# Performance work log

Measured on AMD Instinct MI355X. Metric: run time of the kernel, lower is better.

Reference implementation:

```python
import jax, jax.numpy as jnp
import numpy as np

NC = 6            # CPAB tessellation cells (tess_size=6, zero_boundary=True)
DIM = NC - 1      # theta dimension = 5
SIG_LEN = 2048
CHANNELS = 3
BATCH = 256
FC_IN = 64 * 168  # flattened net_part1 output for signal_len=2048
NUM_SCALING = 0   # N in transform_data_ss
EPS_BN = 1e-5


def _cpab_basis():
    """QR null-space basis of the CPAB continuity + zero-boundary constraints.
    Params ordered [a_1,b_1,...,a_NC,b_NC]; v(x)=a_c x + b_c on cell c."""
    nc = NC
    L = np.zeros((nc + 1, 2 * nc))
    for k in range(1, nc):  # continuity at internal knots x_k = k/nc
        xk = k / nc
        L[k - 1, 2 * (k - 1)] = xk
        L[k - 1, 2 * (k - 1) + 1] = 1.0
        L[k - 1, 2 * k] = -xk
        L[k - 1, 2 * k + 1] = -1.0
    L[nc - 1, 1] = 1.0        # v(0) = 0  -> b_1 = 0
    L[nc, 2 * (nc - 1)] = 1.0  # v(1) = 0 -> a_nc + b_nc = 0
    L[nc, 2 * nc - 1] = 1.0
    Q, _ = np.linalg.qr(L.T, mode='complete')
    return np.ascontiguousarray(Q[:, nc + 1:]).astype(np.float32)  # (12, 5)


def _conv1d(x, w, b):
    y = jax.lax.conv_general_dilated(x, w, (1,), 'VALID',
                                     dimension_numbers=('NCH', 'OIH', 'NCH'))
    return y + b[None, :, None]


def _maxpool1d(x, k, s):
    return jax.lax.reduce_window(x, -jnp.inf, jax.lax.max, (1, 1, k), (1, 1, s), 'VALID')


def _bn(x, g, b, m, v):  # eval-mode BatchNorm1d
    return (x - m[None, :, None]) * (g / jnp.sqrt(v + EPS_BN))[None, :, None] + b[None, :, None]


def _integrate(x, A):
    """Exact CPAB 1D flow integration over t=1 with cell-crossing handling.
    x: (B, n) points in [0,1]; A: (B, NC, 2) per-cell (a, b). Monotone
    trajectories cross at most NC-1 boundaries -> fixed NC+1 iterations."""
    a_all, b_all = A[:, :, 0], A[:, :, 1]
    t = jnp.ones_like(x)
    for _ in range(NC + 1):
        c = jnp.clip(jnp.floor(x * NC).astype(jnp.int32), 0, NC - 1)
        a = jnp.take_along_axis(a_all, c, axis=1)
        b = jnp.take_along_axis(b_all, c, axis=1)
        v = a * x + b
        xb = jnp.where(v >= 0, (c + 1).astype(x.dtype) / NC, c.astype(x.dtype) / NC)
        big_a = jnp.abs(a) > 1e-8
        a_s = jnp.where(big_a, a, 1.0)
        z = x + b / a_s        # shifted coord: x(t) = z*exp(a t) - b/a
        zb = xb + b / a_s
        ratio = zb / jnp.where(jnp.abs(z) > 1e-12, z, 1e-12)
        t_exp = jnp.log(jnp.maximum(ratio, 1e-12)) / a_s
        v_s = jnp.where(jnp.abs(v) > 1e-12, v, 1.0)
        t_lin = (xb - x) / v_s
        thit = jnp.where(big_a, t_exp, t_lin)
        valid = (jnp.abs(v) > 1e-12) & (thit > 0) & (jnp.where(big_a, ratio, 1.0) > 0)
        thit = jnp.where(valid, thit, jnp.inf)
        tau = jnp.minimum(t, thit)
        x_new = jnp.where(big_a, z * jnp.exp(a * tau) - (z - x), x + b * tau)
        hit = thit <= t
        nudge = jnp.where(v >= 0, 1e-6, -1e-6)  # push into next cell
        x = jnp.clip(jnp.where(hit, xb + nudge, x_new), 0.0, 1.0)
        t = jnp.maximum(t - tau, 0.0)
    return x


def _interp1d(data, pos):
    """data: (B, L, C); pos: (B, n) in [0,1] -> (B, n, C) linear interpolation."""
    Lw = data.shape[1]
    p = jnp.clip(pos, 0.0, 1.0) * (Lw - 1)
    x0 = jnp.clip(jnp.floor(p).astype(jnp.int32), 0, Lw - 2)
    w = (p - x0.astype(p.dtype))[:, :, None]
    d0 = jnp.take_along_axis(data, x0[:, :, None], axis=1)
    d1 = jnp.take_along_axis(data, (x0 + 1)[:, :, None], axis=1)
    return d0 * (1.0 - w) + d1 * w


def _transform_data_ss(data, theta, basis, outsize, N):
    """CPAB scaling-and-squaring warp of data (B, L, C) by theta (B, DIM)."""
    Bsz = theta.shape[0]
    A = (theta @ basis.T).reshape(Bsz, NC, 2) / (2.0 ** N)
    grid = jnp.linspace(0.0, 1.0, outsize, dtype=data.dtype)
    grid_t = _integrate(jnp.broadcast_to(grid, (Bsz, outsize)), A)
    for _ in range(N):  # squaring: compose the warp with itself
        grid_t = _interp1d(grid_t[:, :, None], grid_t)[:, :, 0]
    return _interp1d(data, grid_t)


def reference(x, conv1_w, conv1_b, bn1_g, bn1_b, bn1_m, bn1_v,
              conv2_w, conv2_b, bn2_g, bn2_b, bn2_m, bn2_v,
              conv3_w, conv3_b, bn3_g, bn3_b, bn3_m, bn3_v,
              fc1_w, fc1_b, fc2_w, fc2_b, fc3_w, fc3_b, fc4_w, fc4_b, basis):
    # localization net (n_recurrence = 1, back_version = True)
    h = jax.nn.relu(_maxpool1d(_bn(_conv1d(x, conv1_w, conv1_b), bn1_g, bn1_b, bn1_m, bn1_v), 3, 2))
    h = jax.nn.relu(_maxpool1d(_bn(_conv1d(h, conv2_w, conv2_b), bn2_g, bn2_b, bn2_m, bn2_v), 3, 3))
    h = jax.nn.relu(_maxpool1d(_bn(_conv1d(h, conv3_w, conv3_b), bn3_g, bn3_b, bn3_m, bn3_v), 3, 2))
    xs = h.reshape(h.shape[0], -1)  # (B, 64*168)
    xs = jax.nn.relu(xs @ fc1_w.T + fc1_b)
    xs = jax.nn.relu(xs @ fc2_w.T + fc2_b)
    xs = jax.nn.relu(xs @ fc3_w.T + fc3_b)
    theta = jnp.tanh(xs @ fc4_w.T + fc4_b)  # (B, 5)
    data = jnp.transpose(x, (0, 2, 1))       # (B, L, C)
    warped = _transform_data_ss(data, theta, basis, SIG_LEN, NUM_SCALING)
    return jnp.transpose(warped, (0, 2, 1))  # (B, C, L)


def setup_inputs() -> dict:
    key = jax.random.key(0)
    ks = jax.random.split(key, 16)
    def nrm(k, shape, scale):
        return (jax.random.normal(k, shape) * scale).astype(jnp.float32)
    inp = {}
    inp['x'] = jax.random.normal(ks[0], (BATCH, CHANNELS, SIG_LEN), dtype=jnp.float32)
    inp['conv1_w'] = nrm(ks[1], (128, CHANNELS, 3), (CHANNELS * 3) ** -0.5)
    inp['conv1_b'] = nrm(ks[2], (128,), 0.01)
    inp['bn1_g'] = jnp.ones((128,), jnp.float32)
    inp['bn1_b'] = jnp.zeros((128,), jnp.float32)
    inp['bn1_m'] = nrm(ks[3], (128,), 0.1)
    inp['bn1_v'] = jnp.ones((128,), jnp.float32)
    inp['conv2_w'] = nrm(ks[4], (64, 128, 5), (128 * 5) ** -0.5)
    inp['conv2_b'] = nrm(ks[5], (64,), 0.01)
    inp['bn2_g'] = jnp.ones((64,), jnp.float32)
    inp['bn2_b'] = jnp.zeros((64,), jnp.float32)
    inp['bn2_m'] = nrm(ks[6], (64,), 0.1)
    inp['bn2_v'] = jnp.ones((64,), jnp.float32)
    inp['conv3_w'] = nrm(ks[7], (64, 64, 3), (64 * 3) ** -0.5)
    inp['conv3_b'] = nrm(ks[8], (64,), 0.01)
    inp['bn3_g'] = jnp.ones((64,), jnp.float32)
    inp['bn3_b'] = jnp.zeros((64,), jnp.float32)
    inp['bn3_m'] = nrm(ks[9], (64,), 0.1)
    inp['bn3_v'] = jnp.ones((64,), jnp.float32)
    inp['fc1_w'] = nrm(ks[10], (48, FC_IN), FC_IN ** -0.5)
    inp['fc1_b'] = jnp.zeros((48,), jnp.float32)
    inp['fc2_w'] = nrm(ks[11], (32, 48), 48 ** -0.5)
    inp['fc2_b'] = jnp.zeros((32,), jnp.float32)
    inp['fc3_w'] = nrm(ks[12], (16, 32), 32 ** -0.5)
    inp['fc3_b'] = jnp.zeros((16,), jnp.float32)
    # near-identity warp head (original zero-inits weight, identity bias)
    inp['fc4_w'] = nrm(ks[13], (DIM, 16), 0.01)
    inp['fc4_b'] = nrm(ks[14], (DIM,), 0.01)
    inp['basis'] = jnp.asarray(_cpab_basis())
    return inp
```

## Files before the change

kernel.cpp:

```cpp
#include <hip/hip_runtime.h>
#include <math.h>

#define BATCH   256
#define SIGLEN  2048
#define L1OUT   1022
#define L2OUT   339
#define L3OUT   168
#define FCIN    10752

#define TP2   21
#define NROW  68
#define H1S   136

#define TU3   28

typedef float f32x4 __attribute__((ext_vector_type(4)));
typedef short s16x8 __attribute__((ext_vector_type(8)));

__device__ __forceinline__ unsigned short f2bf(float f) {
    unsigned int u = __float_as_uint(f);
    return (unsigned short)((u + 0x7fffu + ((u >> 16) & 1u)) >> 16);
}
__device__ __forceinline__ float bf2f(unsigned short h) {
    return __uint_as_float(((unsigned int)h) << 16);
}

__launch_bounds__(256)
__global__ void prep_kernel(
    const float* __restrict__ conv1_b,
    const float* __restrict__ g1, const float* __restrict__ b1,
    const float* __restrict__ m1, const float* __restrict__ v1,
    const float* __restrict__ conv2_w, const float* __restrict__ conv2_b,
    const float* __restrict__ g2, const float* __restrict__ b2,
    const float* __restrict__ m2, const float* __restrict__ v2,
    const float* __restrict__ conv3_w, const float* __restrict__ conv3_b,
    const float* __restrict__ g3, const float* __restrict__ b3,
    const float* __restrict__ m3, const float* __restrict__ v3,
    const float* __restrict__ fc1_w,
    unsigned short* __restrict__ w2hi, unsigned short* __restrict__ w2lo,
    unsigned short* __restrict__ w3hi, unsigned short* __restrict__ w3lo,
    float* __restrict__ wp1,
    float* __restrict__ so1, float* __restrict__ so2, float* __restrict__ so3)
{
    int tid = blockIdx.x * 256 + threadIdx.x;
    int stride = gridDim.x * 256;
    for (int i = tid; i < 64*128*5; i += stride) {
        int co = i / 640; int rr = i - co*640; int ci = rr / 5; int k = rr - ci*5;
        float w = conv2_w[i];
        unsigned short hi = f2bf(w);
        unsigned short lo = f2bf(w - bf2f(hi));
        int dst = ((k*4 + (ci >> 5))*64 + co)*32 + (ci & 31);
        w2hi[dst] = hi;
        w2lo[dst] = lo;
    }
    for (int i = tid; i < 64*64*3; i += stride) {
        int co = i / 192; int r = i - co*192; int ci = r / 3; int k = r - ci*3;
        float w = conv3_w[i];
        unsigned short hi = f2bf(w);
        unsigned short lo = f2bf(w - bf2f(hi));
        int dst = ((k*2 + (ci >> 5))*64 + co)*32 + (ci & 31);
        w3hi[dst] = hi;
        w3lo[dst] = lo;
    }
    for (int i = tid; i < 48*FCIN; i += stride) {
        int o = i / FCIN; int ph = i - o*FCIN;
        int u = ph >> 6, co = ph & 63;
        wp1[i] = fc1_w[o*FCIN + co*L3OUT + u];
    }
    if (tid < 128) {
        float s = g1[tid] / sqrtf(v1[tid] + 1e-5f);
        so1[tid]       = s;
        so1[128 + tid] = (conv1_b[tid] - m1[tid]) * s + b1[tid];
    }
    if (tid < 64) {
        float s2 = g2[tid] / sqrtf(v2[tid] + 1e-5f);
        so2[tid]      = s2;
        so2[64 + tid] = (conv2_b[tid] - m2[tid]) * s2 + b2[tid];
        float s3 = g3[tid] / sqrtf(v3[tid] + 1e-5f);
        so3[tid]      = s3;
        so3[64 + tid] = (conv3_b[tid] - m3[tid]) * s3 + b3[tid];
    }
}

__launch_bounds__(256, 4)
__global__ void conv12_kernel(
    const float* __restrict__ x, const float* __restrict__ w1,
    const unsigned short* __restrict__ w2hi, const unsigned short* __restrict__ w2lo,
    const float* __restrict__ so1, const float* __restrict__ so2,
    unsigned int* __restrict__ h2p)
{
    __shared__ unsigned short h1hi[NROW * H1S];
    __shared__ unsigned short h1lo[NROW * H1S];

    int t  = threadIdx.x;
    int b  = blockIdx.x;
    int u0 = blockIdx.y * TP2;
    int q0 = 3 * u0;
    int wv = __builtin_amdgcn_readfirstlane(t >> 6);
    int l  = t & 63;
    int m  = l & 15;
    int qd = l >> 4;
    int cp = wv & 1;
    int pp = wv >> 1;

    float wr[2][9];
    float s1r[2], o1r[2];
    #pragma unroll
    for (int h = 0; h < 2; ++h) {
        int ch = l + 64*h;
        #pragma unroll
        for (int j = 0; j < 9; ++j) wr[h][j] = w1[ch*9 + j];
        s1r[h] = so1[ch]; o1r[h] = so1[128 + ch];
    }
    for (int s = 0; s < 17; ++s) {
        int r = 4*s + wv;
        int xbase = 2*(q0 + r);
        float xv[3][5];
        #pragma unroll
        for (int ci = 0; ci < 3; ++ci) {
            const float* xp = x + (b*3 + ci)*SIGLEN;
            #pragma unroll
            for (int d = 0; d < 5; ++d) {
                int xi = xbase + d; xi = xi < SIGLEN ? xi : SIGLEN - 1;
                xv[ci][d] = xp[xi];
            }
        }
        #pragma unroll
        for (int h = 0; h < 2; ++h) {
            float r0 = 0.f, r1 = 0.f, r2 = 0.f;
            #pragma unroll
            for (int ci = 0; ci < 3; ++ci) {
                float wA = wr[h][ci*3], wB = wr[h][ci*3+1], wC = wr[h][ci*3+2];
                r0 = fmaf(xv[ci][0], wA, fmaf(xv[ci][1], wB, fmaf(xv[ci][2], wC, r0)));
                r1 = fmaf(xv[ci][1], wA, fmaf(xv[ci][2], wB, fmaf(xv[ci][3], wC, r1)));
                r2 = fmaf(xv[ci][2], wA, fmaf(xv[ci][3], wB, fmaf(xv[ci][4], wC, r2)));
            }
            float mx = fmaxf(r0, fmaxf(r1, r2));
            float v  = fmaxf(fmaf(s1r[h], mx, o1r[h]), 0.f);
            unsigned short hi = f2bf(v);
            unsigned short lo = f2bf(v - bf2f(hi));
            h1hi[r*H1S + l + 64*h] = hi;
            h1lo[r*H1S + l + 64*h] = lo;
        }
    }
    __syncthreads();

    f32x4 acc[2][2] = {{(f32x4)(0.f), (f32x4)(0.f)}, {(f32x4)(0.f), (f32x4)(0.f)}};

    const unsigned short* whb0 = w2hi + (2*cp  )*512 + m*32 + qd*8;
    const unsigned short* whb1 = w2hi + (2*cp+1)*512 + m*32 + qd*8;
    const unsigned short* wlb0 = w2lo + (2*cp  )*512 + m*32 + qd*8;
    const unsigned short* wlb1 = w2lo + (2*cp+1)*512 + m*32 + qd*8;

    for (int k = 0; k < 5; ++k) {
        #pragma unroll
        for (int cb = 0; cb < 4; ++cb) {
            int st = k*4 + cb;
            s16x8 wh0 = *(const s16x8*)(whb0 + st*2048);
            s16x8 wl0 = *(const s16x8*)(wlb0 + st*2048);
            s16x8 wh1 = *(const s16x8*)(whb1 + st*2048);
            s16x8 wl1 = *(const s16x8*)(wlb1 + st*2048);
            #pragma unroll
            for (int ptl = 0; ptl < 2; ++ptl) {
                int row = (2*pp + ptl)*16 + m + k;
                s16x8 ah = *(const s16x8*)&h1hi[row*H1S + cb*32 + qd*8];
                s16x8 al = *(const s16x8*)&h1lo[row*H1S + cb*32 + qd*8];
                acc[0][ptl] = __builtin_amdgcn_mfma_f32_16x16x32_bf16(ah, wh0, acc[0][ptl], 0, 0, 0);
                acc[0][ptl] = __builtin_amdgcn_mfma_f32_16x16x32_bf16(al, wh0, acc[0][ptl], 0, 0, 0);
                acc[0][ptl] = __builtin_amdgcn_mfma_f32_16x16x32_bf16(ah, wl0, acc[0][ptl], 0, 0, 0);
                acc[1][ptl] = __builtin_amdgcn_mfma_f32_16x16x32_bf16(ah, wh1, acc[1][ptl], 0, 0, 0);
                acc[1][ptl] = __builtin_amdgcn_mfma_f32_16x16x32_bf16(al, wh1, acc[1][ptl], 0, 0, 0);
                acc[1][ptl] = __builtin_amdgcn_mfma_f32_16x16x32_bf16(ah, wl1, acc[1][ptl], 0, 0, 0);
            }
        }
    }
    __syncthreads();

    float* c2 = (float*)h1hi;
    #pragma unroll
    for (int ctl = 0; ctl < 2; ++ctl)
        #pragma unroll
        for (int ptl = 0; ptl < 2; ++ptl)
            #pragma unroll
            for (int rg = 0; rg < 4; ++rg)
                c2[((2*pp + ptl)*16 + qd*4 + rg)*65 + (2*cp + ctl)*16 + m] = acc[ctl][ptl][rg];
    __syncthreads();

    #pragma unroll
    for (int it = 0; it < 6; ++it) {
        int idx = t + it*256;
        if (idx < TP2*64) {
            int ul = idx >> 6, co = idx & 63;
            int u = u0 + ul;
            if (u < L2OUT) {
                float v0 = c2[(3*ul  )*65 + co];
                float v1 = c2[(3*ul+1)*65 + co];
                float v2 = c2[(3*ul+2)*65 + co];
                float mm = fmaxf(v0, fmaxf(v1, v2));
                float v  = fmaxf(fmaf(so2[co], mm, so2[64 + co]), 0.f);
                unsigned short hi = f2bf(v);
                unsigned short lo = f2bf(v - bf2f(hi));
                h2p[(b*L2OUT + u)*64 + co] = (unsigned int)hi | ((unsigned int)lo << 16);
            }
        }
    }
}

__launch_bounds__(256, 4)
__global__ void conv3_kernel(
    const unsigned int* __restrict__ h2p,
    const unsigned short* __restrict__ w3hi, const unsigned short* __restrict__ w3lo,
    const float* __restrict__ so3, float* __restrict__ xs)
{
    __shared__ unsigned short h3hi[66 * 72];
    __shared__ unsigned short h3lo[66 * 72];

    int t  = threadIdx.x;
    int b  = blockIdx.x;
    int u0 = blockIdx.y * TU3;
    int wv = __builtin_amdgcn_readfirstlane(t >> 6);
    int l  = t & 63;
    int m  = l & 15;
    int qd = l >> 4;

    for (int i = t; i < 66*64; i += 256) {
        int r = i >> 6, ci = i & 63;
        int g = 2*u0 + r; g = g > (L2OUT-1) ? (L2OUT-1) : g;
        unsigned int v = h2p[(b*L2OUT + g)*64 + ci];
        h3hi[r*72 + ci] = (unsigned short)(v & 0xffffu);
        h3lo[r*72 + ci] = (unsigned short)(v >> 16);
    }
    __syncthreads();

    s16x8 wh[6], wl[6];
    #pragma unroll
    for (int s = 0; s < 6; ++s) {
        wh[s] = *(const s16x8*)(w3hi + s*2048 + (wv*16 + m)*32 + qd*8);
        wl[s] = *(const s16x8*)(w3lo + s*2048 + (wv*16 + m)*32 + qd*8);
    }

    f32x4 acc[4] = {(f32x4)(0.f), (f32x4)(0.f), (f32x4)(0.f), (f32x4)(0.f)};
    #pragma unroll
    for (int pt = 0; pt < 4; ++pt) {
        #pragma unroll
        for (int s = 0; s < 6; ++s) {
            int row = pt*16 + m + (s >> 1);
            int off = (s & 1)*32 + qd*8;
            s16x8 ah = *(const s16x8*)&h3hi[row*72 + off];
            s16x8 al = *(const s16x8*)&h3lo[row*72 + off];
            acc[pt] = __builtin_amdgcn_mfma_f32_16x16x32_bf16(ah, wh[s], acc[pt], 0, 0, 0);
            acc[pt] = __builtin_amdgcn_mfma_f32_16x16x32_bf16(al, wh[s], acc[pt], 0, 0, 0);
            acc[pt] = __builtin_amdgcn_mfma_f32_16x16x32_bf16(ah, wl[s], acc[pt], 0, 0, 0);
        }
    }
    __syncthreads();

    float* c3 = (float*)h3hi;
    #pragma unroll
    for (int pt = 0; pt < 4; ++pt)
        #pragma unroll
        for (int rg = 0; rg < 4; ++rg)
            c3[(pt*16 + qd*4 + rg)*65 + wv*16 + m] = acc[pt][rg];
    __syncthreads();

    #pragma unroll
    for (int it = 0; it < 7; ++it) {
        int idx = t + it*256;
        if (idx < TU3*64) {
            int ul = idx >> 6, co = idx & 63;
            int p = 2*ul;
            float v0 = c3[(p  )*65 + co];
            float v1 = c3[(p+1)*65 + co];
            float v2 = c3[(p+2)*65 + co];
            float mm = fmaxf(v0, fmaxf(v1, v2));
            xs[b*FCIN + (u0 + ul)*64 + co] = fmaxf(fmaf(so3[co], mm, so3[64 + co]), 0.f);
        }
    }
}

__launch_bounds__(256)
__global__ void fc1_kernel(
    const float* __restrict__ xs, const float* __restrict__ w,
    float* __restrict__ part)
{
    int t = threadIdx.x, lane = t & 63, wid = t >> 6;
    int b0 = blockIdx.x * 4;
    int kc = blockIdx.y;
    int o0 = wid * 12;
    float acc[48];
    #pragma unroll
    for (int i = 0; i < 48; ++i) acc[i] = 0.f;

    int kbase = kc * 1344 + lane;
    for (int ki = 0; ki < 21; ++ki) {
        int k = kbase + ki * 64;
        float xv0 = xs[(b0 + 0) * FCIN + k];
        float xv1 = xs[(b0 + 1) * FCIN + k];
        float xv2 = xs[(b0 + 2) * FCIN + k];
        float xv3 = xs[(b0 + 3) * FCIN + k];
        #pragma unroll
        for (int j = 0; j < 12; ++j) {
            float ww = w[(o0 + j) * FCIN + k];
            acc[j]      += xv0 * ww;
            acc[12 + j] += xv1 * ww;
            acc[24 + j] += xv2 * ww;
            acc[36 + j] += xv3 * ww;
        }
    }
    #pragma unroll
    for (int i = 0; i < 48; ++i) {
        #pragma unroll
        for (int off = 32; off > 0; off >>= 1)
            acc[i] += __shfl_xor(acc[i], off, 64);
    }
    if (lane == 0) {
        #pragma unroll
        for (int bb = 0; bb < 4; ++bb)
            #pragma unroll
            for (int j = 0; j < 12; ++j)
                part[((b0 + bb) * 48 + o0 + j) * 8 + kc] = acc[bb * 12 + j];
    }
}

__launch_bounds__(256)
__global__ void fc234_kernel(
    const float* __restrict__ part, const float* __restrict__ fc1_b,
    const float* __restrict__ fc2_w, const float* __restrict__ fc2_b,
    const float* __restrict__ fc3_w, const float* __restrict__ fc3_b,
    const float* __restrict__ fc4_w, const float* __restrict__ fc4_b,
    const float* __restrict__ basis, float* __restrict__ A)
{
    __shared__ float xsl[256 * 49];
    __shared__ float w2l[1536], w3l[512], w4l[80];
    __shared__ float b2l[32], b3l[16], b4l[8], basl[60];
    int t = threadIdx.x;
    for (int i = t; i < 256 * 48; i += 256) {
        const float4* p = (const float4*)&part[i * 8];
        float4 pa = p[0], pb = p[1];
        float sv = ((pa.x + pa.y) + (pa.z + pa.w)) + ((pb.x + pb.y) + (pb.z + pb.w));
        xsl[(i / 48) * 49 + (i % 48)] = fmaxf(sv + fc1_b[i % 48], 0.f);
    }
    for (int i = t; i < 1536; i += 256) w2l[i] = fc2_w[i];
    for (int i = t; i < 512;  i += 256) w3l[i] = fc3_w[i];
    if (t < 80) w4l[t] = fc4_w[t];
    if (t < 32) b2l[t] = fc2_b[t];
    if (t < 16) b3l[t] = fc3_b[t];
    if (t < 5)  b4l[t] = fc4_b[t];
    if (t < 60) basl[t] = basis[t];
    __syncthreads();

    const float* xin = &xsl[t * 49];
    float h[32];
    #pragma unroll 4
    for (int o = 0; o < 32; ++o) {
        float sv = b2l[o];
        for (int i = 0; i < 48; ++i) sv += w2l[o * 48 + i] * xin[i];
        h[o] = fmaxf(sv, 0.f);
    }
    float g[16];
    #pragma unroll 4
    for (int o = 0; o < 16; ++o) {
        float sv = b3l[o];
        for (int i = 0; i < 32; ++i) sv += w3l[o * 32 + i] * h[i];
        g[o] = fmaxf(sv, 0.f);
    }
    float th[5];
    #pragma unroll
    for (int o = 0; o < 5; ++o) {
        float sv = b4l[o];
        for (int i = 0; i < 16; ++i) sv += w4l[o * 16 + i] * g[i];
        th[o] = tanhf(sv);
    }
    #pragma unroll
    for (int j = 0; j < 12; ++j) {
        float sv = 0.f;
        #pragma unroll
        for (int d = 0; d < 5; ++d) sv += basl[j * 5 + d] * th[d];
        A[t * 12 + j] = sv;
    }
}

__launch_bounds__(256)
__global__ void warp_kernel(
    const float* __restrict__ x, const float* __restrict__ A,
    float* __restrict__ out)
{
    __shared__ float Al[12];
    int b = blockIdx.x;
    int i = blockIdx.y * 256 + threadIdx.x;
    if (threadIdx.x < 12) Al[threadIdx.x] = A[b * 12 + threadIdx.x];
    __syncthreads();

    float xp = (float)i / 2047.f;
    float t  = 1.f;
    for (int it = 0; it < 7; ++it) {
        int c = (int)floorf(xp * 6.f);
        c = min(max(c, 0), 5);
        float a  = Al[2 * c], bb = Al[2 * c + 1];
        float v  = a * xp + bb;
        float xb = (v >= 0.f) ? (float)(c + 1) / 6.f : (float)c / 6.f;
        bool  big_a = fabsf(a) > 1e-8f;
        float a_s = big_a ? a : 1.f;
        float z   = xp + bb / a_s;
        float zb  = xb + bb / a_s;
        float zden = (fabsf(z) > 1e-12f) ? z : 1e-12f;
        float ratio = zb / zden;
        float t_exp = logf(fmaxf(ratio, 1e-12f)) / a_s;
        float v_s   = (fabsf(v) > 1e-12f) ? v : 1.f;
        float t_lin = (xb - xp) / v_s;
        float thit  = big_a ? t_exp : t_lin;
        bool valid  = (fabsf(v) > 1e-12f) && (thit > 0.f) && ((big_a ? ratio : 1.f) > 0.f);
        if (!valid) thit = __builtin_inff();
        float tau   = fminf(t, thit);
        float x_new = big_a ? (z * expf(a * tau) - (z - xp)) : (xp + bb * tau);
        bool hit    = (thit <= t);
        float nudge = (v >= 0.f) ? 1e-6f : -1e-6f;
        xp = hit ? (xb + nudge) : x_new;
        xp = fminf(fmaxf(xp, 0.f), 1.f);
        t  = fmaxf(t - tau, 0.f);
    }
    float p = fminf(fmaxf(xp, 0.f), 1.f) * 2047.f;
    int i0 = (int)floorf(p);
    i0 = min(max(i0, 0), 2046);
    float w = p - (float)i0;
    #pragma unroll
    for (int c = 0; c < 3; ++c) {
        const float* d = &x[(b * 3 + c) * SIGLEN];
        out[(b * 3 + c) * SIGLEN + i] = d[i0] * (1.f - w) + d[i0 + 1] * w;
    }
}

extern "C" void kernel_launch(void* const* d_in, const int* in_sizes, int n_in,
                              void* d_out, int out_size, void* d_ws, size_t ws_size,
                              hipStream_t stream) {
    (void)in_sizes; (void)n_in; (void)out_size; (void)ws_size;
    const float* x       = (const float*)d_in[0];
    const float* conv1_w = (const float*)d_in[1];
    const float* conv1_b = (const float*)d_in[2];
    const float* bn1_g   = (const float*)d_in[3];
    const float* bn1_b   = (const float*)d_in[4];
    const float* bn1_m   = (const float*)d_in[5];
    const float* bn1_v   = (const float*)d_in[6];
    const float* conv2_w = (const float*)d_in[7];
    const float* conv2_b = (const float*)d_in[8];
    const float* bn2_g   = (const float*)d_in[9];
    const float* bn2_b   = (const float*)d_in[10];
    const float* bn2_m   = (const float*)d_in[11];
    const float* bn2_v   = (const float*)d_in[12];
    const float* conv3_w = (const float*)d_in[13];
    const float* conv3_b = (const float*)d_in[14];
    const float* bn3_g   = (const float*)d_in[15];
    const float* bn3_b   = (const float*)d_in[16];
    const float* bn3_m   = (const float*)d_in[17];
    const float* bn3_v   = (const float*)d_in[18];
    const float* fc1_w   = (const float*)d_in[19];
    const float* fc1_b   = (const float*)d_in[20];
    const float* fc2_w   = (const float*)d_in[21];
    const float* fc2_b   = (const float*)d_in[22];
    const float* fc3_w   = (const float*)d_in[23];
    const float* fc3_b   = (const float*)d_in[24];
    const float* fc4_w   = (const float*)d_in[25];
    const float* fc4_b   = (const float*)d_in[26];
    const float* basis   = (const float*)d_in[27];

    unsigned short* w2hi = (unsigned short*)d_ws;
    unsigned short* w2lo = w2hi + 40960;
    unsigned short* w3hi = w2lo + 40960;
    unsigned short* w3lo = w3hi + 12288;
    float* ws   = (float*)d_ws;
    float* so1  = ws + 53248;
    float* so2  = so1 + 256;
    float* so3  = so2 + 128;
    float* wp1  = so3 + 128;
    unsigned int* h2p = (unsigned int*)(wp1 + 516096);
    float* xs   = wp1 + 516096 + 5554176;
    float* part = xs  + 2752512;
    float* Aws  = part + 98304;

    prep_kernel<<<256, 256, 0, stream>>>(
        conv1_b, bn1_g, bn1_b, bn1_m, bn1_v,
        conv2_w, conv2_b, bn2_g, bn2_b, bn2_m, bn2_v,
        conv3_w, conv3_b, bn3_g, bn3_b, bn3_m, bn3_v,
        fc1_w, w2hi, w2lo, w3hi, w3lo, wp1, so1, so2, so3);

    dim3 g2(BATCH, (L2OUT + TP2 - 1) / TP2);
    conv12_kernel<<<g2, 256, 0, stream>>>(x, conv1_w, w2hi, w2lo, so1, so2, h2p);

    dim3 g3(BATCH, L3OUT / TU3);
    conv3_kernel<<<g3, 256, 0, stream>>>(h2p, w3hi, w3lo, so3, xs);

    dim3 gfc(BATCH / 4, 8);
    fc1_kernel<<<gfc, 256, 0, stream>>>(xs, wp1, part);

    fc234_kernel<<<1, 256, 0, stream>>>(part, fc1_b, fc2_w, fc2_b, fc3_w, fc3_b,
                                        fc4_w, fc4_b, basis, Aws);

    dim3 g5(BATCH, SIGLEN / 256);
    warp_kernel<<<g5, 256, 0, stream>>>(x, Aws, (float*)d_out);
}
```

Baseline: 287.3 us.

## Use 32x32x16 MFMA for conv2, split fc1 finer, and simplify fc234

The conv2 weight layout changes so that each wave computes a 32x32 output tile with mfma_f32_32x32x16_bf16 instead of four 16x16x32 tiles, which cuts the number of MFMA issues and LDS fragment loads. The fc1 weight permutation now writes its output in a scattered pattern but reads fc1_w contiguously. The fc1 K-split grows from 8 to 12 chunks to launch more blocks. The single-block fc234 kernel drops its shared-memory weight staging, reads weights straight from global memory with fully unrolled FMAs, and keeps inputs in registers, which raises register pressure.

```diff
diff --git a/kernel.cpp b/kernel.cpp
--- a/kernel.cpp
+++ b/kernel.cpp
@@ -14,8 +14,12 @@
 
 #define TU3   28
 
-typedef float f32x4 __attribute__((ext_vector_type(4)));
-typedef short s16x8 __attribute__((ext_vector_type(8)));
+#define KC1   12
+#define KCL   (FCIN/KC1)
+
+typedef float f32x4  __attribute__((ext_vector_type(4)));
+typedef float f32x16 __attribute__((ext_vector_type(16)));
+typedef short s16x8  __attribute__((ext_vector_type(8)));
 
 __device__ __forceinline__ unsigned short f2bf(float f) {
     unsigned int u = __float_as_uint(f);
@@ -49,7 +53,8 @@
         float w = conv2_w[i];
         unsigned short hi = f2bf(w);
         unsigned short lo = f2bf(w - bf2f(hi));
-        int dst = ((k*4 + (ci >> 5))*64 + co)*32 + (ci & 31);
+        int seg = k*8 + (ci >> 4);
+        int dst = ((seg*2 + (co >> 5))*32 + (co & 31))*16 + (ci & 15);
         w2hi[dst] = hi;
         w2lo[dst] = lo;
     }
@@ -63,9 +68,9 @@
         w3lo[dst] = lo;
     }
     for (int i = tid; i < 48*FCIN; i += stride) {
-        int o = i / FCIN; int ph = i - o*FCIN;
-        int u = ph >> 6, co = ph & 63;
-        wp1[i] = fc1_w[o*FCIN + co*L3OUT + u];
+        int o = i / FCIN; int r = i - o*FCIN;
+        int co = r / L3OUT, u = r - co*L3OUT;
+        wp1[o*FCIN + u*64 + co] = fc1_w[i];
     }
     if (tid < 128) {
         float s = g1[tid] / sqrtf(v1[tid] + 1e-5f);
@@ -98,10 +103,6 @@
     int q0 = 3 * u0;
     int wv = __builtin_amdgcn_readfirstlane(t >> 6);
     int l  = t & 63;
-    int m  = l & 15;
-    int qd = l >> 4;
-    int cp = wv & 1;
-    int pp = wv >> 1;
 
     float wr[2][9];
     float s1r[2], o1r[2];
@@ -145,45 +146,37 @@
     }
     __syncthreads();
 
-    f32x4 acc[2][2] = {{(f32x4)(0.f), (f32x4)(0.f)}, {(f32x4)(0.f), (f32x4)(0.f)}};
-
-    const unsigned short* whb0 = w2hi + (2*cp  )*512 + m*32 + qd*8;
-    const unsigned short* whb1 = w2hi + (2*cp+1)*512 + m*32 + qd*8;
-    const unsigned short* wlb0 = w2lo + (2*cp  )*512 + m*32 + qd*8;
-    const unsigned short* wlb1 = w2lo + (2*cp+1)*512 + m*32 + qd*8;
-
-    for (int k = 0; k < 5; ++k) {
-        #pragma unroll
-        for (int cb = 0; cb < 4; ++cb) {
-            int st = k*4 + cb;
-            s16x8 wh0 = *(const s16x8*)(whb0 + st*2048);
-            s16x8 wl0 = *(const s16x8*)(wlb0 + st*2048);
-            s16x8 wh1 = *(const s16x8*)(whb1 + st*2048);
-            s16x8 wl1 = *(const s16x8*)(wlb1 + st*2048);
-            #pragma unroll
-            for (int ptl = 0; ptl < 2; ++ptl) {
-                int row = (2*pp + ptl)*16 + m + k;
-                s16x8 ah = *(const s16x8*)&h1hi[row*H1S + cb*32 + qd*8];
-                s16x8 al = *(const s16x8*)&h1lo[row*H1S + cb*32 + qd*8];
-                acc[0][ptl] = __builtin_amdgcn_mfma_f32_16x16x32_bf16(ah, wh0, acc[0][ptl], 0, 0, 0);
-                acc[0][ptl] = __builtin_amdgcn_mfma_f32_16x16x32_bf16(al, wh0, acc[0][ptl], 0, 0, 0);
-                acc[0][ptl] = __builtin_amdgcn_mfma_f32_16x16x32_bf16(ah, wl0, acc[0][ptl], 0, 0, 0);
-                acc[1][ptl] = __builtin_amdgcn_mfma_f32_16x16x32_bf16(ah, wh1, acc[1][ptl], 0, 0, 0);
-                acc[1][ptl] = __builtin_amdgcn_mfma_f32_16x16x32_bf16(al, wh1, acc[1][ptl], 0, 0, 0);
-                acc[1][ptl] = __builtin_amdgcn_mfma_f32_16x16x32_bf16(ah, wl1, acc[1][ptl], 0, 0, 0);
-            }
+    int ph  = wv >> 1;
+    int chf = wv & 1;
+    int r32 = l & 31;
+    int oct = l >> 5;
+
+    f32x16 acc = (f32x16)(0.f);
+    const unsigned short* whB = w2hi + (chf*32 + r32)*16 + oct*8;
+    const unsigned short* wlB = w2lo + (chf*32 + r32)*16 + oct*8;
+
+    for (int ks = 0; ks < 5; ++ks) {
+        #pragma unroll
+        for (int cb = 0; cb < 8; ++cb) {
+            int seg = ks*8 + cb;
+            s16x8 wh = *(const s16x8*)(whB + seg*1024);
+            s16x8 wl = *(const s16x8*)(wlB + seg*1024);
+            int row = ph*32 + r32 + ks;
+            s16x8 ah = *(const s16x8*)&h1hi[row*H1S + cb*16 + oct*8];
+            s16x8 al = *(const s16x8*)&h1lo[row*H1S + cb*16 + oct*8];
+            acc = __builtin_amdgcn_mfma_f32_32x32x16_bf16(ah, wh, acc, 0, 0, 0);
+            acc = __builtin_amdgcn_mfma_f32_32x32x16_bf16(al, wh, acc, 0, 0, 0);
+            acc = __builtin_amdgcn_mfma_f32_32x32x16_bf16(ah, wl, acc, 0, 0, 0);
         }
     }
     __syncthreads();
 
     float* c2 = (float*)h1hi;
     #pragma unroll
-    for (int ctl = 0; ctl < 2; ++ctl)
-        #pragma unroll
-        for (int ptl = 0; ptl < 2; ++ptl)
-            #pragma unroll
-            for (int rg = 0; rg < 4; ++rg)
-                c2[((2*pp + ptl)*16 + qd*4 + rg)*65 + (2*cp + ctl)*16 + m] = acc[ctl][ptl][rg];
+    for (int rg = 0; rg < 16; ++rg) {
+        int row = (rg & 3) + 8*(rg >> 2) + 4*oct;
+        c2[(ph*32 + row)*65 + chf*32 + r32] = acc[rg];
+    }
     __syncthreads();
 
     #pragma unroll
@@ -291,8 +284,8 @@
     #pragma unroll
     for (int i = 0; i < 48; ++i) acc[i] = 0.f;
 
-    int kbase = kc * 1344 + lane;
-    for (int ki = 0; ki < 21; ++ki) {
+    int kbase = kc * KCL + lane;
+    for (int ki = 0; ki < KCL/64; ++ki) {
         int k = kbase + ki * 64;
         float xv0 = xs[(b0 + 0) * FCIN + k];
         float xv1 = xs[(b0 + 1) * FCIN + k];
@@ -318,7 +311,7 @@
         for (int bb = 0; bb < 4; ++bb)
             #pragma unroll
             for (int j = 0; j < 12; ++j)
-                part[((b0 + bb) * 48 + o0 + j) * 8 + kc] = acc[bb * 12 + j];
+                part[((b0 + bb) * 48 + o0 + j) * KC1 + kc] = acc[bb * 12 + j];
     }
 }
 
@@ -331,51 +324,48 @@
     const float* __restrict__ basis, float* __restrict__ A)
 {
     __shared__ float xsl[256 * 49];
-    __shared__ float w2l[1536], w3l[512], w4l[80];
-    __shared__ float b2l[32], b3l[16], b4l[8], basl[60];
     int t = threadIdx.x;
     for (int i = t; i < 256 * 48; i += 256) {
-        const float4* p = (const float4*)&part[i * 8];
-        float4 pa = p[0], pb = p[1];
-        float sv = ((pa.x + pa.y) + (pa.z + pa.w)) + ((pb.x + pb.y) + (pb.z + pb.w));
+        const float4* p = (const float4*)&part[i * KC1];
+        float4 pa = p[0], pb = p[1], pc = p[2];
+        float sv = ((pa.x + pa.y) + (pa.z + pa.w))
+                 + ((pb.x + pb.y) + (pb.z + pb.w))
+                 + ((pc.x + pc.y) + (pc.z + pc.w));
         xsl[(i / 48) * 49 + (i % 48)] = fmaxf(sv + fc1_b[i % 48], 0.f);
     }
-    for (int i = t; i < 1536; i += 256) w2l[i] = fc2_w[i];
-    for (int i = t; i < 512;  i += 256) w3l[i] = fc3_w[i];
-    if (t < 80) w4l[t] = fc4_w[t];
-    if (t < 32) b2l[t] = fc2_b[t];
-    if (t < 16) b3l[t] = fc3_b[t];
-    if (t < 5)  b4l[t] = fc4_b[t];
-    if (t < 60) basl[t] = basis[t];
-    __syncthreads();
-
-    const float* xin = &xsl[t * 49];
+    __syncthreads();
+
+    float xin[48];
+    #pragma unroll
+    for (int i = 0; i < 48; ++i) xin[i] = xsl[t * 49 + i];
+
     float h[32];
-    #pragma unroll 4
     for (int o = 0; o < 32; ++o) {
-        float sv = b2l[o];
-        for (int i = 0; i < 48; ++i) sv += w2l[o * 48 + i] * xin[i];
+        float sv = fc2_b[o];
+        #pragma unroll
+        for (int i = 0; i < 48; ++i) sv = fmaf(fc2_w[o * 48 + i], xin[i], sv);
         h[o] = fmaxf(sv, 0.f);
     }
     float g[16];
-    #pragma unroll 4
     for (int o = 0; o < 16; ++o) {
-        float sv = b3l[o];
-        for (int i = 0; i < 32; ++i) sv += w3l[o * 32 + i] * h[i];
+        float sv = fc3_b[o];
+        #pragma unroll
+        for (int i = 0; i < 32; ++i) sv = fmaf(fc3_w[o * 32 + i], h[i], sv);
         g[o] = fmaxf(sv, 0.f);
     }
     float th[5];
     #pragma unroll
     for (int o = 0; o < 5; ++o) {
-        float sv = b4l[o];
-        for (int i = 0; i < 16; ++i) sv += w4l[o * 16 + i] * g[i];
+        float sv = fc4_b[o];
+        #pragma unroll
+        for (int i = 0; i < 16; ++i) sv = fmaf(fc4_w[o * 16 + i], g[i], sv);
         th[o] = tanhf(sv);
     }
     #pragma unroll
     for (int j = 0; j < 12; ++j) {
         float sv = 0.f;
         #pragma unroll
-        for (int d = 0; d < 5; ++d) sv += basl[j * 5 + d] * th[d];
+        for (int d = 0; d < 5; ++d) sv = fmaf(basis[j * 5 + d], th[d], sv);
         A[t * 12 + j] = sv;
     }
 }
@@ -475,7 +465,7 @@
     unsigned int* h2p = (unsigned int*)(wp1 + 516096);
     float* xs   = wp1 + 516096 + 5554176;
     float* part = xs  + 2752512;
-    float* Aws  = part + 98304;
+    float* Aws  = part + 147456;
 
     prep_kernel<<<256, 256, 0, stream>>>(
         conv1_b, bn1_g, bn1_b, bn1_m, bn1_v,
@@ -489,7 +479,7 @@
     dim3 g3(BATCH, L3OUT / TU3);
     conv3_kernel<<<g3, 256, 0, stream>>>(h2p, w3hi, w3lo, so3, xs);
 
-    dim3 gfc(BATCH / 4, 8);
+    dim3 gfc(BATCH / 4, KC1);
     fc1_kernel<<<gfc, 256, 0, stream>>>(xs, wp1, part);
 
     fc234_kernel<<<1, 256, 0, stream>>>(part, fc1_b, fc2_w, fc2_b, fc3_w, fc3_b,
```

Measured after the change: 294.4 us. 1.02x slower.
